# Optimization experiments

Hardware: AMD Instinct MI355X
Metric: run time of the kernel (lower is better)

Reference implementation:

```python
import jax, jax.numpy as jnp
import numpy as np

DIM = 16
HID = 128
B = 1024
STEPS = 10  # RK4 steps in differentiable_forward


def setup_inputs() -> dict:
    key = jax.random.key(0)
    ks = jax.random.split(key, 8)

    def lin(k, fan_in, fan_out):
        return jax.random.normal(k, (fan_in, fan_out), jnp.float32) / np.float32(np.sqrt(fan_in))

    W0 = lin(ks[0], DIM + 1, HID)
    W1 = lin(ks[1], HID, HID)
    W2 = lin(ks[2], HID, HID)
    W3 = lin(ks[3], HID, HID)
    W4 = lin(ks[4], HID, DIM)
    b0 = jnp.zeros((HID,), jnp.float32)
    b1 = jnp.zeros((HID,), jnp.float32)
    b2 = jnp.zeros((HID,), jnp.float32)
    b3 = jnp.zeros((HID,), jnp.float32)
    b4 = jnp.zeros((DIM,), jnp.float32)
    x = jax.random.normal(ks[5], (B, DIM), jnp.float32)
    x_star = jax.random.normal(ks[6], (B, DIM), jnp.float32)
    return dict(x=x, x_star=x_star, W0=W0, b0=b0, W1=W1, b1=b1,
                W2=W2, b2=b2, W3=W3, b3=b3, W4=W4, b4=b4)


def reference(x, x_star, W0, b0, W1, b1, W2, b2, W3, b3, W4, b4):
    dtype = x.dtype

    def vel(t, z):
        # z: [..., DIM]; append scalar time channel -> [..., DIM+1]
        tcol = jnp.full(z.shape[:-1] + (1,), t, dtype)
        h = jnp.concatenate([z, tcol], axis=-1)
        h = jnp.tanh(h @ W0 + b0)
        h = jnp.tanh(h @ W1 + b1)
        h = jnp.tanh(h @ W2 + b2)
        h = jnp.tanh(h @ W3 + b3)
        return h @ W4 + b4

    def flow(z):
        # RK4 integration of the velocity field from t=0 to t=1 (10 steps)
        dt = 1.0 / STEPS
        for i in range(STEPS):
            t = i * dt
            k1 = vel(t, z)
            k2 = vel(t + 0.5 * dt, z + 0.5 * dt * k1)
            k3 = vel(t + 0.5 * dt, z + 0.5 * dt * k2)
            k4 = vel(t + dt, z + dt * k3)
            z = z + (k1 + 2.0 * k2 + 2.0 * k3 + k4) * (dt / 6.0)
        return z

    n = x.shape[0]
    y_comb = flow(jnp.concatenate([x, x_star], axis=0))
    y, y_star = y_comb[:n], y_comb[n:]

    diff = y - y_star
    norm = jnp.linalg.norm(diff, axis=1, keepdims=True) + 1e-8
    grad_phi_y = diff / norm  # [B, DIM]

    # Per-sample Jacobian J[b, i, j] = d y_i / d x_j (flow is pointwise per row)
    J = jax.vmap(jax.jacfwd(flow))(x)  # [B, DIM, DIM]

    G = jnp.einsum('bij,bik->bjk', J, J)  # J^T J
    G_inv = jnp.linalg.inv(G + 1e-6 * jnp.eye(DIM, dtype=dtype))
    grad_phi_x = jnp.einsum('bij,bi->bj', J, grad_phi_y)  # J^T grad_phi_y
    x_dot = -jnp.einsum('bjk,bk->bj', G_inv, grad_phi_x)
    return x_dot
```

## Files before the change

kernel.cpp:

```cpp
#include <hip/hip_runtime.h>
#include <math.h>

typedef _Float16 half8  __attribute__((ext_vector_type(8)));
typedef _Float16 half4  __attribute__((ext_vector_type(4)));
typedef __fp16   fp16x2 __attribute__((ext_vector_type(2)));
typedef float    float4v __attribute__((ext_vector_type(4)));
typedef unsigned uint4v  __attribute__((ext_vector_type(4)));
typedef unsigned uint2v  __attribute__((ext_vector_type(2)));

#define NDIM   16
#define HID    128
#define NSTEP  10
#define RPW    2
#define NROWS  48
#define XSTR   136
#define XISTR  40
#define SBS    17

__device__ __forceinline__ float tanh_fast(float v) {
  float e = __expf(2.f * v);
  return 1.f - 2.f * __builtin_amdgcn_rcpf(e + 1.f);
}

template<int CTRL>
__device__ __forceinline__ float qbcast(float v) {
  int i = __builtin_amdgcn_update_dpp(0, __builtin_bit_cast(int, v), CTRL, 0xF, 0xF, true);
  return __builtin_bit_cast(float, i);
}

__device__ __forceinline__ unsigned pk2(float a, float b) {
  fp16x2 h = __builtin_amdgcn_cvt_pkrtz(a, b);
  return __builtin_bit_cast(unsigned, h);
}
__device__ __forceinline__ half8 h8pack(float a, float b, float c, float d,
                                        float e, float f, float g, float h) {
  uint4v u; u[0] = pk2(a,b); u[1] = pk2(c,d); u[2] = pk2(e,f); u[3] = pk2(g,h);
  return __builtin_bit_cast(half8, u);
}
__device__ __forceinline__ half4 h4pack(float a, float b, float c, float d) {
  uint2v u; u[0] = pk2(a,b); u[1] = pk2(c,d);
  return __builtin_bit_cast(half4, u);
}

__device__ __forceinline__ int oneuron(int c) {
  return 32*(c >> 5) + 16*((c >> 2) & 1) + 4*((c >> 3) & 3) + (c & 3);
}

__global__ __launch_bounds__(256, 2)
void flow_ode_kernel(const float* __restrict__ gx,  const float* __restrict__ gxs,
                     const float* __restrict__ W0,  const float* __restrict__ b0,
                     const float* __restrict__ W1,  const float* __restrict__ b1,
                     const float* __restrict__ W2,  const float* __restrict__ b2,
                     const float* __restrict__ W3,  const float* __restrict__ b3,
                     const float* __restrict__ W4,  const float* __restrict__ b4,
                     float* __restrict__ out)
{
  __shared__ __align__(16) _Float16 XT[2][NROWS][XSTR];
  __shared__ __align__(16) _Float16 XI[NROWS][XISTR];
  __shared__ float SbL[NROWS][SBS];

  const int tid  = threadIdx.x;
  const int mi   = tid >> 6;
  const int lane = tid & 63;
  const int q    = lane >> 4;
  const int ln   = lane & 15;
  const int g0   = blockIdx.x * RPW;

  half8 A0[2];
  half8 A1[2][4], A2[2][4], A3[2][4];
  half8 A4[4];
  float bw[4][2][4];
  float b4r[4];

  #pragma unroll
  for (int mt = 0; mt < 2; ++mt) {
    const int m = 16*(2*mi + mt) + ln;
    #pragma unroll
    for (int j = 0; j < 8; ++j) {
      const int k = 8*q + j;
      A0[mt][j] = (k < NDIM+1) ? (_Float16)W0[k*HID + m] : (_Float16)0.f;
    }
    #pragma unroll
    for (int ks = 0; ks < 4; ++ks) {
      #pragma unroll
      for (int j = 0; j < 8; ++j) {
        const int k = oneuron(32*ks + 8*q + j);
        A1[mt][ks][j] = (_Float16)W1[k*HID + m];
        A2[mt][ks][j] = (_Float16)W2[k*HID + m];
        A3[mt][ks][j] = (_Float16)W3[k*HID + m];
      }
    }
  }
  #pragma unroll
  for (int ks = 0; ks < 4; ++ks)
    #pragma unroll
    for (int j = 0; j < 8; ++j)
      A4[ks][j] = (_Float16)W4[oneuron(32*ks + 8*q + j)*NDIM + ln];

  #pragma unroll
  for (int mt = 0; mt < 2; ++mt)
    #pragma unroll
    for (int r = 0; r < 4; ++r) {
      const int m = 16*(2*mi + mt) + 4*q + r;
      bw[0][mt][r] = b0[m];
      bw[1][mt][r] = b1[m];
      bw[2][mt][r] = b2[m];
      bw[3][mt][r] = b3[m];
    }
  #pragma unroll
  for (int r = 0; r < 4; ++r) b4r[r] = b4[4*q + r];

  float sbr[4], sar[4];
  if (mi == 0) {
    const int p = ln & 3;
    const float* src = (p < 2) ? (gx + (g0 + p)*NDIM) : (gxs + (g0 + p - 2)*NDIM);
    #pragma unroll
    for (int r = 0; r < 4; ++r) sbr[r] = src[4*q + r];
  } else {
    #pragma unroll
    for (int r = 0; r < 4; ++r) sbr[r] = (ln == 4*q + r) ? 1.f : 0.f;
  }
  #pragma unroll
  for (int r = 0; r < 4; ++r) sar[r] = 0.f;

  for (int idx = tid; idx < NROWS*32; idx += 256)
    XI[idx >> 5][idx & 31] = (_Float16)0.f;
  __syncthreads();
  if (mi < 3) {
    half4 x4;
    #pragma unroll
    for (int r = 0; r < 4; ++r) x4[r] = (_Float16)sbr[r];
    *(half4*)&XI[mi*16 + ln][4*q] = x4;
  }
  __syncthreads();

  if (blockIdx.x & 1) __builtin_amdgcn_s_sleep(22);

  const float dt = 1.f / NSTEP;

  auto finish = [&](float4v (&D)[2][3], int wb) {
    float hs[2][4], ss[2][4];
    #pragma unroll
    for (int mt = 0; mt < 2; ++mt)
      #pragma unroll
      for (int r = 0; r < 4; ++r) {
        const float h = tanh_fast(D[mt][0][r]);
        hs[mt][r] = h;
        ss[mt][r] = 1.f - h*h;
      }
    *(half8*)&XT[wb][ln][32*mi + 8*q] =
        h8pack(hs[0][0], hs[0][1], hs[0][2], hs[0][3],
               hs[1][0], hs[1][1], hs[1][2], hs[1][3]);
    float t1v[2][4], t2v[2][4];
    #pragma unroll
    for (int mt = 0; mt < 2; ++mt)
      #pragma unroll
      for (int r = 0; r < 4; ++r) {
        t1v[mt][r] = D[mt][1][r] * qbcast<0x00>(ss[mt][r]);
        t2v[mt][r] = D[mt][2][r] * qbcast<0x55>(ss[mt][r]);
      }
    *(half8*)&XT[wb][16 + ln][32*mi + 8*q] =
        h8pack(t1v[0][0], t1v[0][1], t1v[0][2], t1v[0][3],
               t1v[1][0], t1v[1][1], t1v[1][2], t1v[1][3]);
    *(half8*)&XT[wb][32 + ln][32*mi + 8*q] =
        h8pack(t2v[0][0], t2v[0][1], t2v[0][2], t2v[0][3],
               t2v[1][0], t2v[1][1], t2v[1][2], t2v[1][3]);
    __syncthreads();
  };

  auto mid_layer = [&](const half8 (&A)[2][4], const float (&bb)[2][4], int rb, int wb) {
    float4v D[2][3];
    #pragma unroll
    for (int mt = 0; mt < 2; ++mt)
      #pragma unroll
      for (int nt = 0; nt < 3; ++nt)
        #pragma unroll
        for (int e = 0; e < 4; ++e) D[mt][nt][e] = (nt == 0) ? bb[mt][e] : 0.f;
    #pragma unroll
    for (int ks = 0; ks < 4; ++ks) {
      half8 Bf[3];
      #pragma unroll
      for (int nt = 0; nt < 3; ++nt)
        Bf[nt] = *(const half8*)&XT[rb][nt*16 + ln][32*ks + 8*q];
      #pragma unroll
      for (int nt = 0; nt < 3; ++nt) {
        D[0][nt] = __builtin_amdgcn_mfma_f32_16x16x32_f16(A[0][ks], Bf[nt], D[0][nt], 0, 0, 0);
        D[1][nt] = __builtin_amdgcn_mfma_f32_16x16x32_f16(A[1][ks], Bf[nt], D[1][nt], 0, 0, 0);
      }
    }
    finish(D, wb);
  };

  #pragma unroll 1
  for (int step = 0; step < NSTEP; ++step) {
    const float t0 = step * dt;
    #pragma unroll
    for (int stage = 0; stage < 4; ++stage) {
      {
        float4v D[2][3];
        #pragma unroll
        for (int mt = 0; mt < 2; ++mt)
          #pragma unroll
          for (int nt = 0; nt < 3; ++nt)
            #pragma unroll
            for (int e = 0; e < 4; ++e) D[mt][nt][e] = (nt == 0) ? bw[0][mt][e] : 0.f;
        half8 Bf[3];
        #pragma unroll
        for (int nt = 0; nt < 3; ++nt)
          Bf[nt] = *(const half8*)&XI[nt*16 + ln][8*q];
        #pragma unroll
        for (int nt = 0; nt < 3; ++nt) {
          D[0][nt] = __builtin_amdgcn_mfma_f32_16x16x32_f16(A0[0], Bf[nt], D[0][nt], 0, 0, 0);
          D[1][nt] = __builtin_amdgcn_mfma_f32_16x16x32_f16(A0[1], Bf[nt], D[1][nt], 0, 0, 0);
        }
        finish(D, 0);
      }
      mid_layer(A1, bw[1], 0, 1);
      mid_layer(A2, bw[2], 1, 0);
      mid_layer(A3, bw[3], 0, 1);
      {
        if (mi < 3) {
          float4v Da;
          #pragma unroll
          for (int e = 0; e < 4; ++e) Da[e] = (mi == 0) ? b4r[e] : 0.f;
          #pragma unroll
          for (int ks = 0; ks < 4; ++ks) {
            half8 Ba = *(const half8*)&XT[1][mi*16 + ln][32*ks + 8*q];
            Da = __builtin_amdgcn_mfma_f32_16x16x32_f16(A4[ks], Ba, Da, 0, 0, 0);
          }
          const float c_s = (stage < 2) ? 0.5f*dt : dt;
          half4 xn;
          if (stage < 3) {
            const float w_s = (stage == 0) ? 1.f : 2.f;
            float xv[4];
            #pragma unroll
            for (int r = 0; r < 4; ++r) {
              sar[r] += w_s * Da[r];
              xv[r] = sbr[r] + c_s * Da[r];
            }
            xn = h4pack(xv[0], xv[1], xv[2], xv[3]);
          } else {
            float xv[4];
            #pragma unroll
            for (int r = 0; r < 4; ++r) {
              const float nb = sbr[r] + (dt * (1.f/6.f)) * (sar[r] + Da[r]);
              sbr[r] = nb;
              sar[r] = 0.f;
              xv[r] = nb;
            }
            xn = h4pack(xv[0], xv[1], xv[2], xv[3]);
          }
          *(half4*)&XI[mi*16 + ln][4*q] = xn;
          if (mi == 0 && q == 0)
            XI[ln][16] = (_Float16)(t0 + ((stage < 2) ? 0.5f*dt : dt));
        }
        __syncthreads();
      }
    }
  }

  if (mi < 3) {
    #pragma unroll
    for (int r = 0; r < 4; ++r)
      SbL[mi*16 + ln][4*q + r] = sbr[r];
  }
  __syncthreads();

  if (mi < RPW) {
    const int p    = mi;
    const int jj   = ln;
    const int base = lane & 48;
    float c[NDIM], gv[NDIM], G[NDIM];
    #pragma unroll
    for (int i = 0; i < NDIM; ++i) c[i] = SbL[16 + 16*p + jj][i];
    float n2 = 0.f;
    #pragma unroll
    for (int i = 0; i < NDIM; ++i) {
      gv[i] = SbL[p][i] - SbL[2 + p][i];
      n2 += gv[i]*gv[i];
    }
    const float rinv = 1.f / (sqrtf(n2) + 1e-8f);
    float rhs = 0.f;
    #pragma unroll
    for (int i = 0; i < NDIM; ++i) rhs += c[i] * gv[i];
    rhs *= rinv;
    #pragma unroll
    for (int k = 0; k < NDIM; ++k) {
      float acc = (k == jj) ? 1e-6f : 0.f;
      #pragma unroll
      for (int i = 0; i < NDIM; ++i)
        acc += c[i] * __shfl(c[i], base + k, 64);
      G[k] = acc;
    }
    #pragma unroll
    for (int k = 0; k < NDIM-1; ++k) {
      const float piv  = __shfl(G[k], base + k, 64);
      const float prhs = __shfl(rhs,  base + k, 64);
      const float f = (jj > k) ? G[k] / piv : 0.f;
      #pragma unroll
      for (int cc = k; cc < NDIM; ++cc)
        G[cc] -= f * __shfl(G[cc], base + k, 64);
      rhs -= f * prhs;
    }
    float sol = 0.f;
    #pragma unroll
    for (int k = NDIM-1; k >= 0; --k) {
      const float piv = __shfl(G[k], base + k, 64);
      const float pr  = __shfl(rhs,  base + k, 64);
      const float xk  = pr / piv;
      if (jj == k) sol = xk;
      if (jj <  k) rhs -= G[k] * xk;
    }
    if (lane < NDIM)
      out[(g0 + p)*NDIM + jj] = -sol;
  }
}

extern "C" void kernel_launch(void* const* d_in, const int* in_sizes, int n_in,
                              void* d_out, int out_size, void* d_ws, size_t ws_size,
                              hipStream_t stream) {
  (void)in_sizes; (void)n_in; (void)d_ws; (void)ws_size; (void)out_size;
  flow_ode_kernel<<<dim3(512), dim3(256), 0, stream>>>(
      (const float*)d_in[0],  (const float*)d_in[1],
      (const float*)d_in[2],  (const float*)d_in[3],
      (const float*)d_in[4],  (const float*)d_in[5],
      (const float*)d_in[6],  (const float*)d_in[7],
      (const float*)d_in[8],  (const float*)d_in[9],
      (const float*)d_in[10], (const float*)d_in[11],
      (float*)d_out);
}
```

Measured before the change: 224.0 us.

## Compute output layer redundantly per wave and feed layer 0 via register permutes

```diff
diff --git a/kernel.cpp b/kernel.cpp
--- a/kernel.cpp
+++ b/kernel.cpp
@@ -6,7 +6,6 @@
 typedef __fp16   fp16x2 __attribute__((ext_vector_type(2)));
 typedef float    float4v __attribute__((ext_vector_type(4)));
 typedef unsigned uint4v  __attribute__((ext_vector_type(4)));
-typedef unsigned uint2v  __attribute__((ext_vector_type(2)));
 
 #define NDIM   16
 #define HID    128
@@ -14,7 +13,6 @@
 #define RPW    2
 #define NROWS  48
 #define XSTR   136
-#define XISTR  40
 #define SBS    17
 
 __device__ __forceinline__ float tanh_fast(float v) {
@@ -36,10 +34,6 @@
                                         float e, float f, float g, float h) {
   uint4v u; u[0] = pk2(a,b); u[1] = pk2(c,d); u[2] = pk2(e,f); u[3] = pk2(g,h);
   return __builtin_bit_cast(half8, u);
-}
-__device__ __forceinline__ half4 h4pack(float a, float b, float c, float d) {
-  uint2v u; u[0] = pk2(a,b); u[1] = pk2(c,d);
-  return __builtin_bit_cast(half4, u);
 }
 
 __device__ __forceinline__ int oneuron(int c) {
@@ -56,7 +50,6 @@
                      float* __restrict__ out)
 {
   __shared__ __align__(16) _Float16 XT[2][NROWS][XSTR];
-  __shared__ __align__(16) _Float16 XI[NROWS][XISTR];
   __shared__ float SbL[NROWS][SBS];
 
   const int tid  = threadIdx.x;
@@ -110,31 +103,19 @@
   #pragma unroll
   for (int r = 0; r < 4; ++r) b4r[r] = b4[4*q + r];
 
-  float sbr[4], sar[4];
-  if (mi == 0) {
+  float sbr[3][4], sar[3][4];
+  {
     const int p = ln & 3;
     const float* src = (p < 2) ? (gx + (g0 + p)*NDIM) : (gxs + (g0 + p - 2)*NDIM);
     #pragma unroll
-    for (int r = 0; r < 4; ++r) sbr[r] = src[4*q + r];
-  } else {
-    #pragma unroll
-    for (int r = 0; r < 4; ++r) sbr[r] = (ln == 4*q + r) ? 1.f : 0.f;
-  }
-  #pragma unroll
-  for (int r = 0; r < 4; ++r) sar[r] = 0.f;
-
-  for (int idx = tid; idx < NROWS*32; idx += 256)
-    XI[idx >> 5][idx & 31] = (_Float16)0.f;
-  __syncthreads();
-  if (mi < 3) {
-    half4 x4;
-    #pragma unroll
-    for (int r = 0; r < 4; ++r) x4[r] = (_Float16)sbr[r];
-    *(half4*)&XI[mi*16 + ln][4*q] = x4;
-  }
-  __syncthreads();
-
-  if (blockIdx.x & 1) __builtin_amdgcn_s_sleep(22);
+    for (int r = 0; r < 4; ++r) {
+      sbr[0][r] = src[4*q + r];
+      const float e = (ln == 4*q + r) ? 1.f : 0.f;
+      sbr[1][r] = e;
+      sbr[2][r] = e;
+      sar[0][r] = 0.f; sar[1][r] = 0.f; sar[2][r] = 0.f;
+    }
+  }
 
   const float dt = 1.f / NSTEP;
 
@@ -191,78 +172,103 @@
     finish(D, wb);
   };
 
+  auto l0_from_regs = [&](float (&xn)[3][4], float tn) {
+    const int s0 = ((lane & 48) << 1) + (lane & 15);
+    uint4v bfu[3];
+    #pragma unroll
+    for (int nt = 0; nt < 3; ++nt) {
+      const int lo = (int)pk2(xn[nt][0], xn[nt][1]);
+      const int hi = (int)pk2(xn[nt][2], xn[nt][3]);
+      unsigned u0 = (unsigned)__builtin_amdgcn_ds_bpermute(s0 << 2, lo);
+      unsigned u1 = (unsigned)__builtin_amdgcn_ds_bpermute(s0 << 2, hi);
+      unsigned u2 = (unsigned)__builtin_amdgcn_ds_bpermute((s0 + 16) << 2, lo);
+      unsigned u3 = (unsigned)__builtin_amdgcn_ds_bpermute((s0 + 16) << 2, hi);
+      if (q == 2) { u0 = (nt == 0) ? pk2(tn, 0.f) : 0u; u1 = 0u; u2 = 0u; u3 = 0u; }
+      if (q == 3) { u0 = 0u; u1 = 0u; u2 = 0u; u3 = 0u; }
+      bfu[nt][0] = u0; bfu[nt][1] = u1; bfu[nt][2] = u2; bfu[nt][3] = u3;
+    }
+    float4v D[2][3];
+    #pragma unroll
+    for (int mt = 0; mt < 2; ++mt)
+      #pragma unroll
+      for (int nt = 0; nt < 3; ++nt)
+        #pragma unroll
+        for (int e = 0; e < 4; ++e) D[mt][nt][e] = (nt == 0) ? bw[0][mt][e] : 0.f;
+    #pragma unroll
+    for (int nt = 0; nt < 3; ++nt) {
+      half8 Bf = __builtin_bit_cast(half8, bfu[nt]);
+      D[0][nt] = __builtin_amdgcn_mfma_f32_16x16x32_f16(A0[0], Bf, D[0][nt], 0, 0, 0);
+      D[1][nt] = __builtin_amdgcn_mfma_f32_16x16x32_f16(A0[1], Bf, D[1][nt], 0, 0, 0);
+    }
+    finish(D, 0);
+  };
+
+  {
+    float xn0[3][4];
+    #pragma unroll
+    for (int nt = 0; nt < 3; ++nt)
+      #pragma unroll
+      for (int r = 0; r < 4; ++r) xn0[nt][r] = sbr[nt][r];
+    l0_from_regs(xn0, 0.f);
+  }
+
+  if (blockIdx.x & 1) __builtin_amdgcn_s_sleep(22);
+
   #pragma unroll 1
   for (int step = 0; step < NSTEP; ++step) {
     const float t0 = step * dt;
     #pragma unroll
     for (int stage = 0; stage < 4; ++stage) {
-      {
-        float4v D[2][3];
-        #pragma unroll
-        for (int mt = 0; mt < 2; ++mt)
-          #pragma unroll
-          for (int nt = 0; nt < 3; ++nt)
-            #pragma unroll
-            for (int e = 0; e < 4; ++e) D[mt][nt][e] = (nt == 0) ? bw[0][mt][e] : 0.f;
-        half8 Bf[3];
-        #pragma unroll
-        for (int nt = 0; nt < 3; ++nt)
-          Bf[nt] = *(const half8*)&XI[nt*16 + ln][8*q];
-        #pragma unroll
-        for (int nt = 0; nt < 3; ++nt) {
-          D[0][nt] = __builtin_amdgcn_mfma_f32_16x16x32_f16(A0[0], Bf[nt], D[0][nt], 0, 0, 0);
-          D[1][nt] = __builtin_amdgcn_mfma_f32_16x16x32_f16(A0[1], Bf[nt], D[1][nt], 0, 0, 0);
-        }
-        finish(D, 0);
-      }
       mid_layer(A1, bw[1], 0, 1);
       mid_layer(A2, bw[2], 1, 0);
       mid_layer(A3, bw[3], 0, 1);
       {
-        if (mi < 3) {
-          float4v Da;
+        float4v Da[3];
+        #pragma unroll
+        for (int nt = 0; nt < 3; ++nt)
           #pragma unroll
-          for (int e = 0; e < 4; ++e) Da[e] = (mi == 0) ? b4r[e] : 0.f;
+          for (int e = 0; e < 4; ++e) Da[nt][e] = (nt == 0) ? b4r[e] : 0.f;
+        #pragma unroll
+        for (int ks = 0; ks < 4; ++ks) {
           #pragma unroll
-          for (int ks = 0; ks < 4; ++ks) {
-            half8 Ba = *(const half8*)&XT[1][mi*16 + ln][32*ks + 8*q];
-            Da = __builtin_amdgcn_mfma_f32_16x16x32_f16(A4[ks], Ba, Da, 0, 0, 0);
+          for (int nt = 0; nt < 3; ++nt) {
+            half8 Ba = *(const half8*)&XT[1][nt*16 + ln][32*ks + 8*q];
+            Da[nt] = __builtin_amdgcn_mfma_f32_16x16x32_f16(A4[ks], Ba, Da[nt], 0, 0, 0);
           }
-          const float c_s = (stage < 2) ? 0.5f*dt : dt;
-          half4 xn;
-          if (stage < 3) {
-            const float w_s = (stage == 0) ? 1.f : 2.f;
-            float xv[4];
+        }
+        const float c_s = (stage < 2) ? 0.5f*dt : dt;
+        const float tn  = t0 + c_s;
+        float xn[3][4];
+        if (stage < 3) {
+          const float w_s = (stage == 0) ? 1.f : 2.f;
+          #pragma unroll
+          for (int nt = 0; nt < 3; ++nt)
             #pragma unroll
             for (int r = 0; r < 4; ++r) {
-              sar[r] += w_s * Da[r];
-              xv[r] = sbr[r] + c_s * Da[r];
+              sar[nt][r] += w_s * Da[nt][r];
+              xn[nt][r] = sbr[nt][r] + c_s * Da[nt][r];
             }
-            xn = h4pack(xv[0], xv[1], xv[2], xv[3]);
-          } else {
-            float xv[4];
+        } else {
+          #pragma unroll
+          for (int nt = 0; nt < 3; ++nt)
             #pragma unroll
             for (int r = 0; r < 4; ++r) {
-              const float nb = sbr[r] + (dt * (1.f/6.f)) * (sar[r] + Da[r]);
-              sbr[r] = nb;
-              sar[r] = 0.f;
-              xv[r] = nb;
+              sbr[nt][r] += (dt * (1.f/6.f)) * (sar[nt][r] + Da[nt][r]);
+              sar[nt][r] = 0.f;
+              xn[nt][r] = sbr[nt][r];
             }
-            xn = h4pack(xv[0], xv[1], xv[2], xv[3]);
-          }
-          *(half4*)&XI[mi*16 + ln][4*q] = xn;
-          if (mi == 0 && q == 0)
-            XI[ln][16] = (_Float16)(t0 + ((stage < 2) ? 0.5f*dt : dt));
         }
-        __syncthreads();
-      }
-    }
-  }
-
-  if (mi < 3) {
-    #pragma unroll
-    for (int r = 0; r < 4; ++r)
-      SbL[mi*16 + ln][4*q + r] = sbr[r];
+        l0_from_regs(xn, tn);
+      }
+    }
+  }
+
+  if (mi == 0) {
+    #pragma unroll
+    for (int nt = 0; nt < 3; ++nt)
+      #pragma unroll
+      for (int r = 0; r < 4; ++r)
+        SbL[nt*16 + ln][4*q + r] = sbr[nt][r];
   }
   __syncthreads();
 
```

After: 248.6 us. +11.0%, slower.
